# Kernel tuning notes

Hardware: AMD Instinct MI355X
Metric: run time of the kernel (lower is better)

## Reference

```python
import jax, jax.numpy as jnp
import numpy as np

DIM = 1024
HEADS = 16
SCALE = DIM ** -0.5  # NOTE: original scales by full dim, not head dim


def setup_inputs() -> dict:
    key = jax.random.key(0)
    ks = jax.random.split(key, 6)
    B, S, D = 2, 2048, DIM
    x = jax.random.normal(ks[0], (B, S, D), dtype=jnp.float32)
    Wq = jax.random.normal(ks[1], (D, D), dtype=jnp.float32) * 0.02
    Wk = jax.random.normal(ks[2], (D, D), dtype=jnp.float32) * 0.02
    Wv = jax.random.normal(ks[3], (D, D), dtype=jnp.float32) * 0.02
    Wo = jax.random.normal(ks[4], (D, D), dtype=jnp.float32) * 0.02
    z = jnp.zeros((D,), dtype=jnp.float32)
    return {"x": x, "Wq": Wq, "bq": z, "Wk": Wk, "bk": z, "Wv": Wv, "bv": z, "Wo": Wo, "bo": z}


def reference(x, Wq, bq, Wk, bk, Wv, bv, Wo, bo):
    B, S, D = x.shape
    H = HEADS
    d = D // H
    # projections (Linear: x @ W + b)
    q = (x @ Wq + bq).reshape(B, S, H, d).transpose(0, 2, 1, 3)  # b h i d
    k = (x @ Wk + bk).reshape(B, S, H, d).transpose(0, 2, 1, 3)  # b h j d
    v = (x @ Wv + bv).reshape(B, S, H, d).transpose(0, 2, 1, 3)  # b h j d
    dots = jnp.einsum("bhid,bhjd->bhij", q, k) * SCALE
    # causal mask: strict upper triangle -> -inf
    mask = jnp.triu(jnp.ones((S, S), dtype=bool), k=1)
    dots = jnp.where(mask, -jnp.inf, dots)
    attn = jax.nn.softmax(dots, axis=-1)
    out = jnp.einsum("bhij,bhjd->bhid", attn, v)
    out = out.transpose(0, 2, 1, 3).reshape(B, S, D)  # b i (h d)
    return out @ Wo + bo
```

## Files before the change

### kernel.cpp

```cpp
#include <hip/hip_runtime.h>
#include <hip/hip_bf16.h>

typedef __bf16 bf16;
typedef __bf16 bf16x4 __attribute__((ext_vector_type(4)));
typedef __bf16 bf16x8 __attribute__((ext_vector_type(8)));
typedef float floatx4 __attribute__((ext_vector_type(4)));

#define MFMA_16x16x32(a, b, c) __builtin_amdgcn_mfma_f32_16x16x32_bf16((a), (b), (c), 0, 0, 0)
#define NEG_INF (-__builtin_inff())

#define CB 2
#define CS 2048
#define CD 1024
#define CH 16
#define CM (CB * CS)
#define QSC (0.03125f * 1.44269504088896340736f)

__device__ __forceinline__ void async16(const bf16* g, bf16* l) {
    __builtin_amdgcn_global_load_lds(
        (const __attribute__((address_space(1))) void*)g,
        (__attribute__((address_space(3))) void*)l, 16, 0, 0);
}

__global__ __launch_bounds__(256) void conv_x(const float* __restrict__ x,
                                              bf16* __restrict__ xb) {
    size_t i = ((size_t)blockIdx.x * 256 + threadIdx.x) * 8;
    float4 a = *(const float4*)(x + i);
    float4 b = *(const float4*)(x + i + 4);
    bf16x8 v;
    v[0] = (bf16)a.x; v[1] = (bf16)a.y; v[2] = (bf16)a.z; v[3] = (bf16)a.w;
    v[4] = (bf16)b.x; v[5] = (bf16)b.y; v[6] = (bf16)b.z; v[7] = (bf16)b.w;
    *(bf16x8*)(xb + i) = v;
}

__global__ __launch_bounds__(256) void conv_wt(
    const float* __restrict__ W0, const float* __restrict__ W1,
    const float* __restrict__ W2, const float* __restrict__ W3,
    bf16* __restrict__ Wt) {
    __shared__ bf16 Ws[64 * 68];
    const float* W = blockIdx.z == 0 ? W0 : blockIdx.z == 1 ? W1
                   : blockIdx.z == 2 ? W2 : W3;
    bf16* out = Wt + (size_t)blockIdx.z * CD * CD;
    const int t = threadIdx.x;
    const int n0 = blockIdx.x * 64, k0 = blockIdx.y * 64;
    const int rr = t >> 4, c4 = (t & 15) * 4;
#pragma unroll
    for (int i = 0; i < 4; i++) {
        int r = rr + i * 16;
        float4 f = *(const float4*)(W + (size_t)(k0 + r) * CD + n0 + c4);
        bf16x4 v;
        v[0] = (bf16)f.x; v[1] = (bf16)f.y; v[2] = (bf16)f.z; v[3] = (bf16)f.w;
        *(bf16x4*)&Ws[r * 68 + c4] = v;
    }
    __syncthreads();
#pragma unroll
    for (int i = 0; i < 4; i++) {
        int n = rr + i * 16;
        bf16x4 v;
#pragma unroll
        for (int j = 0; j < 4; j++) v[j] = Ws[(c4 + j) * 68 + n];
        *(bf16x4*)(out + (size_t)(n0 + n) * CD + k0 + c4) = v;
    }
}

__global__ __launch_bounds__(256) void gemm_qkv(
    const bf16* __restrict__ A, const bf16* __restrict__ Bt,
    const float* __restrict__ bq, const float* __restrict__ bk,
    const float* __restrict__ bv,
    bf16* __restrict__ Qb, bf16* __restrict__ Kb, bf16* __restrict__ Vb) {
    __shared__ bf16 As[2][128 * 32];
    __shared__ bf16 Bs[2][128 * 32];
    const int t = threadIdx.x, w = t >> 6, lane = t & 63;
    const int quad = lane >> 4, l15 = lane & 15;
    const int which = blockIdx.x >> 3;
    const int bn = (blockIdx.x & 7) * 128, bm = blockIdx.y * 128;
    const bf16* Bw = Bt + (size_t)which * CD * CD;
    const bool vpath = (which == 2);

    const bf16* ag = A + (size_t)(bm + w * 16 + (lane >> 2)) * CD + (lane & 3) * 8;
    const bf16* bg = Bw + (size_t)(bn + w * 16 + (lane >> 2)) * CD + (lane & 3) * 8;
    const int lo = w * 16 * 32;

    const int wm = (w >> 1) * 64, wn = (w & 1) * 64;
    floatx4 acc[4][4] = {};

    for (int k0 = 0; k0 < CD; k0 += 64) {
        async16(ag + k0,                      &As[0][lo]);
        async16(ag + (size_t)64 * CD + k0,    &As[0][lo + 64 * 32]);
        async16(ag + k0 + 32,                 &As[1][lo]);
        async16(ag + (size_t)64 * CD + k0 + 32, &As[1][lo + 64 * 32]);
        async16(bg + k0,                      &Bs[0][lo]);
        async16(bg + (size_t)64 * CD + k0,    &Bs[0][lo + 64 * 32]);
        async16(bg + k0 + 32,                 &Bs[1][lo]);
        async16(bg + (size_t)64 * CD + k0 + 32, &Bs[1][lo + 64 * 32]);
        __syncthreads();
#pragma unroll
        for (int s = 0; s < 2; s++) {
            bf16x8 af[4], bfr[4];
#pragma unroll
            for (int mt = 0; mt < 4; mt++)
                af[mt] = *(const bf16x8*)&As[s][(wm + mt * 16 + l15) * 32 + quad * 8];
#pragma unroll
            for (int nt = 0; nt < 4; nt++)
                bfr[nt] = *(const bf16x8*)&Bs[s][(wn + nt * 16 + l15) * 32 + quad * 8];
            if (vpath) {
#pragma unroll
                for (int mt = 0; mt < 4; mt++)
#pragma unroll
                    for (int nt = 0; nt < 4; nt++)
                        acc[mt][nt] = MFMA_16x16x32(af[mt], bfr[nt], acc[mt][nt]);
            } else {
#pragma unroll
                for (int mt = 0; mt < 4; mt++)
#pragma unroll
                    for (int nt = 0; nt < 4; nt++)
                        acc[mt][nt] = MFMA_16x16x32(bfr[nt], af[mt], acc[mt][nt]);
            }
        }
        __syncthreads();
    }

    if (vpath) {
#pragma unroll
        for (int mt = 0; mt < 4; mt++)
#pragma unroll
            for (int nt = 0; nt < 4; nt++) {
                int token = bm + wm + mt * 16 + quad * 4;
                int col = bn + wn + nt * 16 + l15;
                int b = token >> 11, s = token & (CS - 1);
                int h = col >> 6, dd = col & 63;
                bf16x4 pv;
#pragma unroll
                for (int r = 0; r < 4; r++) pv[r] = (bf16)(acc[mt][nt][r] + bv[col]);
                *(bf16x4*)&Vb[(((size_t)(b * CH + h)) * 64 + dd) * CS + s] = pv;
            }
    } else {
        const float* bias = which == 0 ? bq : bk;
        bf16* out = which == 0 ? Qb : Kb;
#pragma unroll
        for (int mt = 0; mt < 4; mt++)
#pragma unroll
            for (int nt = 0; nt < 4; nt++) {
                int token = bm + wm + mt * 16 + l15;
                int f = bn + wn + nt * 16 + quad * 4;
                int b = token >> 11, s = token & (CS - 1);
                int h = f >> 6, dd = f & 63;
                float4 bb = *(const float4*)(bias + f);
                bf16x4 pv;
#pragma unroll
                for (int r = 0; r < 4; r++) {
                    float v = acc[mt][nt][r] + ((const float*)&bb)[r];
                    if (which == 0) v *= QSC;
                    pv[r] = (bf16)v;
                }
                *(bf16x4*)&out[(((size_t)(b * CH + h)) * CS + s) * 64 + dd] = pv;
            }
    }
}

__global__ __launch_bounds__(256) void gemm_o(
    const bf16* __restrict__ A, const bf16* __restrict__ Bt,
    const float* __restrict__ bias, float* __restrict__ out) {
    __shared__ bf16 As[2][64 * 32];
    __shared__ bf16 Bs[2][128 * 32];
    const int t = threadIdx.x, w = t >> 6, lane = t & 63;
    const int quad = lane >> 4, l15 = lane & 15;
    const int bn = blockIdx.x * 128, bm = blockIdx.y * 64;

    const bf16* ag = A + (size_t)(bm + w * 16 + (lane >> 2)) * CD + (lane & 3) * 8;
    const bf16* bg = Bt + (size_t)(bn + w * 16 + (lane >> 2)) * CD + (lane & 3) * 8;
    const int lo = w * 16 * 32;

    const int wm = (w >> 1) * 32, wn = (w & 1) * 64;
    floatx4 acc[2][4] = {};

    for (int k0 = 0; k0 < CD; k0 += 64) {
        async16(ag + k0,                        &As[0][lo]);
        async16(ag + k0 + 32,                   &As[1][lo]);
        async16(bg + k0,                        &Bs[0][lo]);
        async16(bg + (size_t)64 * CD + k0,      &Bs[0][lo + 64 * 32]);
        async16(bg + k0 + 32,                   &Bs[1][lo]);
        async16(bg + (size_t)64 * CD + k0 + 32, &Bs[1][lo + 64 * 32]);
        __syncthreads();
#pragma unroll
        for (int s = 0; s < 2; s++) {
            bf16x8 af[2], bfr[4];
#pragma unroll
            for (int mt = 0; mt < 2; mt++)
                af[mt] = *(const bf16x8*)&As[s][(wm + mt * 16 + l15) * 32 + quad * 8];
#pragma unroll
            for (int nt = 0; nt < 4; nt++)
                bfr[nt] = *(const bf16x8*)&Bs[s][(wn + nt * 16 + l15) * 32 + quad * 8];
#pragma unroll
            for (int mt = 0; mt < 2; mt++)
#pragma unroll
                for (int nt = 0; nt < 4; nt++)
                    acc[mt][nt] = MFMA_16x16x32(bfr[nt], af[mt], acc[mt][nt]);
        }
        __syncthreads();
    }

#pragma unroll
    for (int mt = 0; mt < 2; mt++)
#pragma unroll
        for (int nt = 0; nt < 4; nt++) {
            int token = bm + wm + mt * 16 + l15;
            int f = bn + wn + nt * 16 + quad * 4;
            float4 bb = *(const float4*)(bias + f);
            float4 ov;
            ov.x = acc[mt][nt][0] + bb.x;
            ov.y = acc[mt][nt][1] + bb.y;
            ov.z = acc[mt][nt][2] + bb.z;
            ov.w = acc[mt][nt][3] + bb.w;
            *(float4*)&out[(size_t)token * CD + f] = ov;
        }
}

__global__ __launch_bounds__(256) void attn_kernel(
    const bf16* __restrict__ Q, const bf16* __restrict__ Kg,
    const bf16* __restrict__ Vg, bf16* __restrict__ Ob) {
    __shared__ bf16 Ks[64 * 72];
    __shared__ bf16 Vt[64 * 72];
    __shared__ bf16 Pt[4][32 * 72];

    const int t = threadIdx.x;
    const int w = t >> 6, lane = t & 63;
    const int quad = lane >> 4, l15 = lane & 15;

    const int half = blockIdx.x >> 8;
    const int slot = blockIdx.x & 255;
    const int bh   = slot & 31;
    const int qq   = slot >> 5;
    const int qb   = half ? qq : (15 - qq);
    const int q0   = qb * 128;
    const int wrow0 = q0 + w * 32;
    const int nT = 2 * qb + 2;

    const bf16* Qh = Q + (size_t)bh * CS * 64;
    const bf16* Kh = Kg + (size_t)bh * CS * 64;
    const bf16* Vh = Vg + (size_t)bh * 64 * CS;

    const int strow = t >> 2, soff = (t & 3) * 16;
    const bf16* ksrc = Kh + (size_t)strow * 64 + soff;
    const bf16* vsrc = Vh + (size_t)strow * CS + soff;

    bf16x8 kr0 = *(const bf16x8*)ksrc;
    bf16x8 kr1 = *(const bf16x8*)(ksrc + 8);
    bf16x8 vr0 = *(const bf16x8*)vsrc;
    bf16x8 vr1 = *(const bf16x8*)(vsrc + 8);

    bf16x8 qf[2][2];
#pragma unroll
    for (int g = 0; g < 2; g++) {
        const bf16* qsrc = Qh + (size_t)(wrow0 + g * 16 + l15) * 64 + quad * 8;
        qf[g][0] = *(const bf16x8*)qsrc;
        qf[g][1] = *(const bf16x8*)(qsrc + 32);
    }

    floatx4 o[4][2] = {};
    float l_r[2] = {0.f, 0.f};

    bf16x8 ones;
#pragma unroll
    for (int j = 0; j < 8; j++) ones[j] = (bf16)1.0f;

    bf16* pw = Pt[w];

    for (int kt = 0; kt < nT; kt++) {
        const int ks0 = kt * 64;
        __syncthreads();
        *(bf16x8*)&Ks[strow * 72 + soff]     = kr0;
        *(bf16x8*)&Ks[strow * 72 + soff + 8] = kr1;
        *(bf16x8*)&Vt[strow * 72 + soff]     = vr0;
        *(bf16x8*)&Vt[strow * 72 + soff + 8] = vr1;
        __syncthreads();
        {
            int nk = (kt + 1 < nT) ? kt + 1 : 0;
            const bf16* kn = ksrc + (size_t)nk * 64 * 64;
            const bf16* vn = vsrc + nk * 64;
            kr0 = *(const bf16x8*)kn;
            kr1 = *(const bf16x8*)(kn + 8);
            vr0 = *(const bf16x8*)vn;
            vr1 = *(const bf16x8*)(vn + 8);
        }
        if (ks0 > wrow0 + 31) continue;

        floatx4 sc[2][4] = {};
#pragma unroll
        for (int nt = 0; nt < 4; nt++) {
            bf16x8 af0 = *(const bf16x8*)&Ks[(nt * 16 + l15) * 72 + quad * 8];
            bf16x8 af1 = *(const bf16x8*)&Ks[(nt * 16 + l15) * 72 + 32 + quad * 8];
#pragma unroll
            for (int g = 0; g < 2; g++) {
                sc[g][nt] = MFMA_16x16x32(af0, qf[g][0], sc[g][nt]);
                sc[g][nt] = MFMA_16x16x32(af1, qf[g][1], sc[g][nt]);
            }
        }
        if (ks0 + 63 > wrow0) {
#pragma unroll
            for (int g = 0; g < 2; g++) {
                int qrow = wrow0 + g * 16 + l15;
#pragma unroll
                for (int nt = 0; nt < 4; nt++)
#pragma unroll
                    for (int r = 0; r < 4; r++)
                        if (ks0 + nt * 16 + quad * 4 + r > qrow)
                            sc[g][nt][r] = NEG_INF;
            }
        }
#pragma unroll
        for (int g = 0; g < 2; g++)
#pragma unroll
            for (int nt = 0; nt < 4; nt++) {
                bf16x4 pk;
#pragma unroll
                for (int r = 0; r < 4; r++)
                    pk[r] = (bf16)__builtin_amdgcn_exp2f(sc[g][nt][r]);
                *(bf16x4*)&pw[(g * 16 + l15) * 72 + nt * 16 + quad * 4] = pk;
            }
        bf16x8 bp[2][2];
#pragma unroll
        for (int g = 0; g < 2; g++) {
            bp[g][0] = *(const bf16x8*)&pw[(g * 16 + l15) * 72 + quad * 8];
            bp[g][1] = *(const bf16x8*)&pw[(g * 16 + l15) * 72 + 32 + quad * 8];
        }
#pragma unroll
        for (int g = 0; g < 2; g++) {
            floatx4 sr = {};
            sr = MFMA_16x16x32(ones, bp[g][0], sr);
            sr = MFMA_16x16x32(ones, bp[g][1], sr);
            l_r[g] += sr[0];
        }
#pragma unroll
        for (int dt = 0; dt < 4; dt++) {
            bf16x8 av0 = *(const bf16x8*)&Vt[(dt * 16 + l15) * 72 + quad * 8];
            bf16x8 av1 = *(const bf16x8*)&Vt[(dt * 16 + l15) * 72 + 32 + quad * 8];
#pragma unroll
            for (int g = 0; g < 2; g++) {
                o[dt][g] = MFMA_16x16x32(av0, bp[g][0], o[dt][g]);
                o[dt][g] = MFMA_16x16x32(av1, bp[g][1], o[dt][g]);
            }
        }
    }

    const int b = bh >> 4, h = bh & 15;
#pragma unroll
    for (int g = 0; g < 2; g++) {
        float rl = 1.f / l_r[g];
        int row = wrow0 + g * 16 + l15;
#pragma unroll
        for (int dt = 0; dt < 4; dt++) {
            bf16x4 ov;
#pragma unroll
            for (int r = 0; r < 4; r++) ov[r] = (bf16)(o[dt][g][r] * rl);
            *(bf16x4*)&Ob[((size_t)b * CS + row) * CD + h * 64 + dt * 16 + quad * 4] = ov;
        }
    }
}

extern "C" void kernel_launch(void* const* d_in, const int* in_sizes, int n_in,
                              void* d_out, int out_size, void* d_ws, size_t ws_size,
                              hipStream_t stream) {
    const float* x  = (const float*)d_in[0];
    const float* Wq = (const float*)d_in[1];
    const float* bq = (const float*)d_in[2];
    const float* Wk = (const float*)d_in[3];
    const float* bk = (const float*)d_in[4];
    const float* Wv = (const float*)d_in[5];
    const float* bv = (const float*)d_in[6];
    const float* Wo = (const float*)d_in[7];
    const float* bo = (const float*)d_in[8];
    float* out = (float*)d_out;

    bf16* xb = (bf16*)d_ws;
    bf16* Wt = xb + (size_t)CM * CD;
    bf16* Qb = Wt + (size_t)4 * CD * CD;
    bf16* Kb = Qb + (size_t)CB * CH * CS * 64;
    bf16* Vb = Kb + (size_t)CB * CH * CS * 64;
    bf16* Ob = Vb + (size_t)CB * CH * CS * 64;

    conv_x<<<(CM * CD) / (256 * 8), 256, 0, stream>>>(x, xb);
    conv_wt<<<dim3(CD / 64, CD / 64, 4), 256, 0, stream>>>(Wq, Wk, Wv, Wo, Wt);

    gemm_qkv<<<dim3(24, CM / 128), 256, 0, stream>>>(
        xb, Wt, bq, bk, bv, Qb, Kb, Vb);

    attn_kernel<<<512, 256, 0, stream>>>(Qb, Kb, Vb, Ob);

    gemm_o<<<dim3(8, CM / 64), 256, 0, stream>>>(
        Ob, Wt + (size_t)3 * CD * CD, bo, out);
}
```

Measured before the change: 204.8 us.

## Replace async LDS loads with register-prefetched double-buffered tiles, single barrier per step

The two GEMM kernels drop the direct global-to-LDS async loads. They now prefetch the next 32-wide K slice into registers, store it into alternating shared buffers, and use one barrier per step instead of two. The attention kernel also double-buffers its K/V shared tiles so the leading barrier can be removed. The aim is to overlap global loads with MFMA work and cut synchronisation, at the cost of twice as many loop iterations in the GEMMs, extra register pressure and more LDS use in attention.

Result: slower. 214.1 us (+4.6%).

```diff
diff --git a/kernel.cpp b/kernel.cpp
--- a/kernel.cpp
+++ b/kernel.cpp
@@ -15,12 +15,6 @@
 #define CH 16
 #define CM (CB * CS)
 #define QSC (0.03125f * 1.44269504088896340736f)
-
-__device__ __forceinline__ void async16(const bf16* g, bf16* l) {
-    __builtin_amdgcn_global_load_lds(
-        (const __attribute__((address_space(1))) void*)g,
-        (__attribute__((address_space(3))) void*)l, 16, 0, 0);
-}
 
 __global__ __launch_bounds__(256) void conv_x(const float* __restrict__ x,
                                               bf16* __restrict__ xb) {
@@ -77,47 +71,56 @@
     const bf16* Bw = Bt + (size_t)which * CD * CD;
     const bool vpath = (which == 2);
 
-    const bf16* ag = A + (size_t)(bm + w * 16 + (lane >> 2)) * CD + (lane & 3) * 8;
-    const bf16* bg = Bw + (size_t)(bn + w * 16 + (lane >> 2)) * CD + (lane & 3) * 8;
-    const int lo = w * 16 * 32;
+    const int srow = t >> 2;
+    const int selem = (t & 3) * 8;
+    const bf16* agp  = A + (size_t)(bm + srow) * CD + selem;
+    const bf16* agp2 = agp + (size_t)64 * CD;
+    const bf16* bgp  = Bw + (size_t)(bn + srow) * CD + selem;
+    const bf16* bgp2 = bgp + (size_t)64 * CD;
+
+    bf16x8 ar0 = *(const bf16x8*)agp;
+    bf16x8 ar1 = *(const bf16x8*)agp2;
+    bf16x8 br0 = *(const bf16x8*)bgp;
+    bf16x8 br1 = *(const bf16x8*)bgp2;
 
     const int wm = (w >> 1) * 64, wn = (w & 1) * 64;
     floatx4 acc[4][4] = {};
 
-    for (int k0 = 0; k0 < CD; k0 += 64) {
-        async16(ag + k0,                      &As[0][lo]);
-        async16(ag + (size_t)64 * CD + k0,    &As[0][lo + 64 * 32]);
-        async16(ag + k0 + 32,                 &As[1][lo]);
-        async16(ag + (size_t)64 * CD + k0 + 32, &As[1][lo + 64 * 32]);
-        async16(bg + k0,                      &Bs[0][lo]);
-        async16(bg + (size_t)64 * CD + k0,    &Bs[0][lo + 64 * 32]);
-        async16(bg + k0 + 32,                 &Bs[1][lo]);
-        async16(bg + (size_t)64 * CD + k0 + 32, &Bs[1][lo + 64 * 32]);
+    for (int i = 0; i < 32; i++) {
+        bf16* as = As[i & 1];
+        bf16* bs = Bs[i & 1];
+        *(bf16x8*)&as[srow * 32 + selem]        = ar0;
+        *(bf16x8*)&as[(srow + 64) * 32 + selem] = ar1;
+        *(bf16x8*)&bs[srow * 32 + selem]        = br0;
+        *(bf16x8*)&bs[(srow + 64) * 32 + selem] = br1;
         __syncthreads();
-#pragma unroll
-        for (int s = 0; s < 2; s++) {
-            bf16x8 af[4], bfr[4];
+        if (i < 31) {
+            const int k0 = (i + 1) * 32;
+            ar0 = *(const bf16x8*)(agp + k0);
+            ar1 = *(const bf16x8*)(agp2 + k0);
+            br0 = *(const bf16x8*)(bgp + k0);
+            br1 = *(const bf16x8*)(bgp2 + k0);
+        }
+        bf16x8 af[4], bfr[4];
+#pragma unroll
+        for (int mt = 0; mt < 4; mt++)
+            af[mt] = *(const bf16x8*)&as[(wm + mt * 16 + l15) * 32 + quad * 8];
+#pragma unroll
+        for (int nt = 0; nt < 4; nt++)
+            bfr[nt] = *(const bf16x8*)&bs[(wn + nt * 16 + l15) * 32 + quad * 8];
+        if (vpath) {
 #pragma unroll
             for (int mt = 0; mt < 4; mt++)
-                af[mt] = *(const bf16x8*)&As[s][(wm + mt * 16 + l15) * 32 + quad * 8];
-#pragma unroll
-            for (int nt = 0; nt < 4; nt++)
-                bfr[nt] = *(const bf16x8*)&Bs[s][(wn + nt * 16 + l15) * 32 + quad * 8];
-            if (vpath) {
-#pragma unroll
-                for (int mt = 0; mt < 4; mt++)
-#pragma unroll
-                    for (int nt = 0; nt < 4; nt++)
-                        acc[mt][nt] = MFMA_16x16x32(af[mt], bfr[nt], acc[mt][nt]);
-            } else {
-#pragma unroll
-                for (int mt = 0; mt < 4; mt++)
-#pragma unroll
-                    for (int nt = 0; nt < 4; nt++)
-                        acc[mt][nt] = MFMA_16x16x32(bfr[nt], af[mt], acc[mt][nt]);
-            }
-        }
-        __syncthreads();
+#pragma unroll
+                for (int nt = 0; nt < 4; nt++)
+                    acc[mt][nt] = MFMA_16x16x32(af[mt], bfr[nt], acc[mt][nt]);
+        } else {
+#pragma unroll
+            for (int mt = 0; mt < 4; mt++)
+#pragma unroll
+                for (int nt = 0; nt < 4; nt++)
+                    acc[mt][nt] = MFMA_16x16x32(bfr[nt], af[mt], acc[mt][nt]);
+        }
     }
 
     if (vpath) {
@@ -167,37 +170,44 @@
     const int quad = lane >> 4, l15 = lane & 15;
     const int bn = blockIdx.x * 128, bm = blockIdx.y * 64;
 
-    const bf16* ag = A + (size_t)(bm + w * 16 + (lane >> 2)) * CD + (lane & 3) * 8;
-    const bf16* bg = Bt + (size_t)(bn + w * 16 + (lane >> 2)) * CD + (lane & 3) * 8;
-    const int lo = w * 16 * 32;
+    const int srow = t >> 2;
+    const int selem = (t & 3) * 8;
+    const bf16* agp  = A + (size_t)(bm + srow) * CD + selem;
+    const bf16* bgp  = Bt + (size_t)(bn + srow) * CD + selem;
+    const bf16* bgp2 = bgp + (size_t)64 * CD;
+
+    bf16x8 ar0 = *(const bf16x8*)agp;
+    bf16x8 br0 = *(const bf16x8*)bgp;
+    bf16x8 br1 = *(const bf16x8*)bgp2;
 
     const int wm = (w >> 1) * 32, wn = (w & 1) * 64;
     floatx4 acc[2][4] = {};
 
-    for (int k0 = 0; k0 < CD; k0 += 64) {
-        async16(ag + k0,                        &As[0][lo]);
-        async16(ag + k0 + 32,                   &As[1][lo]);
-        async16(bg + k0,                        &Bs[0][lo]);
-        async16(bg + (size_t)64 * CD + k0,      &Bs[0][lo + 64 * 32]);
-        async16(bg + k0 + 32,                   &Bs[1][lo]);
-        async16(bg + (size_t)64 * CD + k0 + 32, &Bs[1][lo + 64 * 32]);
+    for (int i = 0; i < 32; i++) {
+        bf16* as = As[i & 1];
+        bf16* bs = Bs[i & 1];
+        *(bf16x8*)&as[srow * 32 + selem]        = ar0;
+        *(bf16x8*)&bs[srow * 32 + selem]        = br0;
+        *(bf16x8*)&bs[(srow + 64) * 32 + selem] = br1;
         __syncthreads();
-#pragma unroll
-        for (int s = 0; s < 2; s++) {
-            bf16x8 af[2], bfr[4];
-#pragma unroll
-            for (int mt = 0; mt < 2; mt++)
-                af[mt] = *(const bf16x8*)&As[s][(wm + mt * 16 + l15) * 32 + quad * 8];
+        if (i < 31) {
+            const int k0 = (i + 1) * 32;
+            ar0 = *(const bf16x8*)(agp + k0);
+            br0 = *(const bf16x8*)(bgp + k0);
+            br1 = *(const bf16x8*)(bgp2 + k0);
+        }
+        bf16x8 af[2], bfr[4];
+#pragma unroll
+        for (int mt = 0; mt < 2; mt++)
+            af[mt] = *(const bf16x8*)&as[(wm + mt * 16 + l15) * 32 + quad * 8];
+#pragma unroll
+        for (int nt = 0; nt < 4; nt++)
+            bfr[nt] = *(const bf16x8*)&bs[(wn + nt * 16 + l15) * 32 + quad * 8];
+#pragma unroll
+        for (int mt = 0; mt < 2; mt++)
 #pragma unroll
             for (int nt = 0; nt < 4; nt++)
-                bfr[nt] = *(const bf16x8*)&Bs[s][(wn + nt * 16 + l15) * 32 + quad * 8];
-#pragma unroll
-            for (int mt = 0; mt < 2; mt++)
-#pragma unroll
-                for (int nt = 0; nt < 4; nt++)
-                    acc[mt][nt] = MFMA_16x16x32(bfr[nt], af[mt], acc[mt][nt]);
-        }
-        __syncthreads();
+                acc[mt][nt] = MFMA_16x16x32(bfr[nt], af[mt], acc[mt][nt]);
     }
 
 #pragma unroll
@@ -219,8 +229,8 @@
 __global__ __launch_bounds__(256) void attn_kernel(
     const bf16* __restrict__ Q, const bf16* __restrict__ Kg,
     const bf16* __restrict__ Vg, bf16* __restrict__ Ob) {
-    __shared__ bf16 Ks[64 * 72];
-    __shared__ bf16 Vt[64 * 72];
+    __shared__ bf16 Ks[2][64 * 72];
+    __shared__ bf16 Vt[2][64 * 72];
     __shared__ bf16 Pt[4][32 * 72];
 
     const int t = threadIdx.x;
@@ -268,11 +278,12 @@
 
     for (int kt = 0; kt < nT; kt++) {
         const int ks0 = kt * 64;
-        __syncthreads();
-        *(bf16x8*)&Ks[strow * 72 + soff]     = kr0;
-        *(bf16x8*)&Ks[strow * 72 + soff + 8] = kr1;
-        *(bf16x8*)&Vt[strow * 72 + soff]     = vr0;
-        *(bf16x8*)&Vt[strow * 72 + soff + 8] = vr1;
+        bf16* ks = Ks[kt & 1];
+        bf16* vt = Vt[kt & 1];
+        *(bf16x8*)&ks[strow * 72 + soff]     = kr0;
+        *(bf16x8*)&ks[strow * 72 + soff + 8] = kr1;
+        *(bf16x8*)&vt[strow * 72 + soff]     = vr0;
+        *(bf16x8*)&vt[strow * 72 + soff + 8] = vr1;
         __syncthreads();
         {
             int nk = (kt + 1 < nT) ? kt + 1 : 0;
@@ -288,8 +299,8 @@
         floatx4 sc[2][4] = {};
 #pragma unroll
         for (int nt = 0; nt < 4; nt++) {
-            bf16x8 af0 = *(const bf16x8*)&Ks[(nt * 16 + l15) * 72 + quad * 8];
-            bf16x8 af1 = *(const bf16x8*)&Ks[(nt * 16 + l15) * 72 + 32 + quad * 8];
+            bf16x8 af0 = *(const bf16x8*)&ks[(nt * 16 + l15) * 72 + quad * 8];
+            bf16x8 af1 = *(const bf16x8*)&ks[(nt * 16 + l15) * 72 + 32 + quad * 8];
 #pragma unroll
             for (int g = 0; g < 2; g++) {
                 sc[g][nt] = MFMA_16x16x32(af0, qf[g][0], sc[g][nt]);
@@ -333,8 +344,8 @@
         }
 #pragma unroll
         for (int dt = 0; dt < 4; dt++) {
-            bf16x8 av0 = *(const bf16x8*)&Vt[(dt * 16 + l15) * 72 + quad * 8];
-            bf16x8 av1 = *(const bf16x8*)&Vt[(dt * 16 + l15) * 72 + 32 + quad * 8];
+            bf16x8 av0 = *(const bf16x8*)&vt[(dt * 16 + l15) * 72 + quad * 8];
+            bf16x8 av1 = *(const bf16x8*)&vt[(dt * 16 + l15) * 72 + 32 + quad * 8];
 #pragma unroll
             for (int g = 0; g < 2; g++) {
                 o[dt][g] = MFMA_16x16x32(av0, bp[g][0], o[dt][g]);
```
